# Kernel optimization log

Measured on AMD Instinct MI355X. Metric: run time of the kernel, lower is better.

Reference implementation:

```python
import jax, jax.numpy as jnp
import numpy as np

DIM_IN = 512
HIDDEN = 512
DIM_OUT = 512
BATCH = 256

def _n_tri(d):
    return (d * d + d) // 2

def _quad_expand(x):
    # x: [B, D] -> [B, D + (D^2+D)/2] with upper-triu (incl diag) pairwise products
    d = x.shape[1]
    iu0, iu1 = np.triu_indices(d)  # static indices
    x_sq = x[:, iu0] * x[:, iu1]  # [B, n_tri] -- avoids materializing full outer
    return jnp.concatenate([x, x_sq], axis=-1)

def setup_inputs() -> dict:
    key = jax.random.key(0)
    k = jax.random.split(key, 5)
    f0 = DIM_IN + _n_tri(DIM_IN)
    f1 = HIDDEN + _n_tri(HIDDEN)
    s0 = 1.0 / np.sqrt(f0)
    s1 = 1.0 / np.sqrt(f1)
    return {
        "x": jax.random.normal(k[0], (BATCH, DIM_IN), dtype=jnp.float32),
        "W0": jax.random.uniform(k[1], (HIDDEN, f0), dtype=jnp.float32, minval=-s0, maxval=s0),
        "b0": jax.random.uniform(k[2], (HIDDEN,), dtype=jnp.float32, minval=-s0, maxval=s0),
        "W1": jax.random.uniform(k[3], (DIM_OUT, f1), dtype=jnp.float32, minval=-s1, maxval=s1),
        "b1": jax.random.uniform(k[4], (DIM_OUT,), dtype=jnp.float32, minval=-s1, maxval=s1),
    }

def reference(x, W0, b0, W1, b1):
    h = _quad_expand(x) @ W0.T + b0  # [B, HIDDEN]
    out = _quad_expand(h) @ W1.T + b1  # [B, DIM_OUT]
    return out
```

## Files before the change

kernel.cpp:

```cpp
#include <hip/hip_runtime.h>

typedef short s16x8 __attribute__((ext_vector_type(8)));
typedef float f32x4 __attribute__((ext_vector_type(4)));

#define DIM     512
#define BATCH   256
#define NTRI    131328
#define FDIM    131840
#define KBLOCKS 2060
#define BN      64
#define NTILES  8
#define CCH     64

__device__ __forceinline__ unsigned short f2bf(float f) {
  __bf16 h = (__bf16)f;
  return __builtin_bit_cast(unsigned short, h);
}
__device__ __forceinline__ float bf2f(unsigned short s) {
  union { unsigned u; float f; } v; v.u = (unsigned)s << 16; return v.f;
}
__device__ __forceinline__ unsigned pk2(float a, float b) {
  return (unsigned)f2bf(a) | ((unsigned)f2bf(b) << 16);
}
__device__ __forceinline__ int swz(int m) { return (m ^ (m >> 2)) & 7; }

__global__ void setup(unsigned* __restrict__ table, const float* __restrict__ x,
                      unsigned short* __restrict__ Xt) {
  int bid = blockIdx.x;
  if (bid < 512) {
    int i = bid;
    int base = i * DIM - (i * (i - 1)) / 2;
    int len = DIM - i;
    for (int t = threadIdx.x; t < len; t += blockDim.x)
      table[base + t] = ((unsigned)i << 16) | (unsigned)(i + t);
  } else {
    int t = (bid - 512) * blockDim.x + threadIdx.x;
    int r = t & (BATCH - 1);
    int c = t >> 8;
    Xt[c * BATCH + r] = f2bf(x[r * DIM + c]);
  }
}

__global__ __launch_bounds__(512)
void featgen(const unsigned* __restrict__ table,
             const unsigned short* __restrict__ Xt,
             uint4* __restrict__ Feat)
{
  const int kb = blockIdx.x;
  const int tid = threadIdx.x;
  const int s8 = tid >> 6;
  const int lane = tid & 63;
  const int f0 = kb * 64 + s8 * 8;
  uint4* out = Feat + ((size_t)kb * 8 + s8) * 256;

  if (f0 < DIM) {
    #pragma unroll
    for (int mb = 0; mb < 4; ++mb) {
      int m = mb * 64 + lane;
      unsigned short v[8];
      #pragma unroll
      for (int e = 0; e < 8; ++e) v[e] = Xt[(f0 + e) * BATCH + m];
      uint4 pk;
      pk.x = (unsigned)v[0] | ((unsigned)v[1] << 16);
      pk.y = (unsigned)v[2] | ((unsigned)v[3] << 16);
      pk.z = (unsigned)v[4] | ((unsigned)v[5] << 16);
      pk.w = (unsigned)v[6] | ((unsigned)v[7] << 16);
      out[m] = pk;
    }
  } else {
    int p0 = f0 - DIM;
    unsigned t0 = table[p0], t7 = table[p0 + 7];
    if ((t0 >> 16) == (t7 >> 16)) {
      int i = (int)(t0 >> 16), j0 = (int)(t0 & 0xffffu);
      #pragma unroll
      for (int mb = 0; mb < 4; ++mb) {
        int m = mb * 64 + lane;
        float xi = bf2f(Xt[i * BATCH + m]);
        float pr[8];
        #pragma unroll
        for (int e = 0; e < 8; ++e) pr[e] = xi * bf2f(Xt[(j0 + e) * BATCH + m]);
        out[m] = make_uint4(pk2(pr[0], pr[1]), pk2(pr[2], pr[3]),
                            pk2(pr[4], pr[5]), pk2(pr[6], pr[7]));
      }
    } else {
      unsigned tt[8];
      #pragma unroll
      for (int e = 0; e < 8; ++e) tt[e] = table[p0 + e];
      #pragma unroll
      for (int mb = 0; mb < 4; ++mb) {
        int m = mb * 64 + lane;
        float pr[8];
        #pragma unroll
        for (int e = 0; e < 8; ++e)
          pr[e] = bf2f(Xt[(tt[e] >> 16) * BATCH + m]) * bf2f(Xt[(tt[e] & 0xffffu) * BATCH + m]);
        out[m] = make_uint4(pk2(pr[0], pr[1]), pk2(pr[2], pr[3]),
                            pk2(pr[4], pr[5]), pk2(pr[6], pr[7]));
      }
    }
  }
}

__global__ __launch_bounds__(512, 4)
void qgemm(const uint4* __restrict__ Feat,
           const float* __restrict__ W,
           unsigned short* __restrict__ partial,
           int C)
{
  __shared__ unsigned short Ws[2][4096];
  const int chunk = blockIdx.x % C;
  const int ntile = blockIdx.x / C;
  const int kb0 = (KBLOCKS * chunk) / C;
  const int kb1 = (KBLOCKS * (chunk + 1)) / C;
  const int n0 = ntile * BN;
  const int tid = threadIdx.x;
  const int lane = tid & 63;
  const int wave = tid >> 6;
  const int lm = lane & 15;
  const int lk = lane >> 4;

  const int wr0 = tid >> 4;
  const int wc16 = tid & 15;

  f32x4 acc[2][4] = {};
  f32x4 wregC[2], wregN[2], wT[2];
  uint4 afrC[2][2], afrN[2][2];

  const float* wp0 = W + (size_t)(n0 + wr0) * FDIM + wc16 * 4;
  const size_t wrow32 = (size_t)32 * FDIM;
  const int abase = lk * 256 + wave * 32 + lm;

  auto loadA = [&](uint4 (*a)[2], int kb) {
    #pragma unroll
    for (int mf = 0; mf < 2; ++mf)
      #pragma unroll
      for (int ks = 0; ks < 2; ++ks)
        a[mf][ks] = Feat[(size_t)kb * 2048 + ks * 1024 + mf * 16 + abase];
  };
  auto loadWr = [&](f32x4* w, int kb) {
    #pragma unroll
    for (int it = 0; it < 2; ++it)
      w[it] = *(const f32x4*)(wp0 + it * wrow32 + (size_t)kb * 64);
  };
  auto storeWs = [&](int buf, const f32x4* w) {
    #pragma unroll
    for (int it = 0; it < 2; ++it) {
      int r = wr0 + it * 32;
      int slot = (wc16 >> 1) ^ swz(r);
      *(uint2*)((char*)&Ws[buf][0] + r * 128 + slot * 16 + (wc16 & 1) * 8) =
          make_uint2(pk2(w[it][0], w[it][1]), pk2(w[it][2], w[it][3]));
    }
  };
  auto compute = [&](int buf, uint4 (*a)[2]) {
    #pragma unroll
    for (int ks = 0; ks < 2; ++ks) {
      s16x8 bfr[4];
      #pragma unroll
      for (int nf = 0; nf < 4; ++nf) {
        int n = nf * 16 + lm;
        int slot = (ks * 4 + lk) ^ swz(n);
        bfr[nf] = *(const s16x8*)((const char*)&Ws[buf][0] + n * 128 + slot * 16);
      }
      __builtin_amdgcn_s_setprio(1);
      #pragma unroll
      for (int mf = 0; mf < 2; ++mf)
        #pragma unroll
        for (int nf = 0; nf < 4; ++nf)
          acc[mf][nf] = __builtin_amdgcn_mfma_f32_16x16x32_bf16(
              __builtin_bit_cast(s16x8, a[mf][ks]), bfr[nf], acc[mf][nf], 0, 0, 0);
      __builtin_amdgcn_s_setprio(0);
    }
  };

  loadA(afrC, kb0);
  loadWr(wT, kb0);
  loadWr(wregC, min(kb0 + 1, KBLOCKS - 1));
  storeWs(kb0 & 1, wT);
  asm volatile("s_waitcnt lgkmcnt(0)" ::: "memory");
  __builtin_amdgcn_s_barrier();

  for (int kb = kb0; kb < kb1 - 1; ++kb) {
    const int buf = kb & 1;
    loadA(afrN, kb + 1);
    loadWr(wregN, min(kb + 2, KBLOCKS - 1));
    storeWs(buf ^ 1, wregC);
    compute(buf, afrC);
    asm volatile("s_waitcnt lgkmcnt(0)" ::: "memory");
    __builtin_amdgcn_s_barrier();
    #pragma unroll
    for (int mf = 0; mf < 2; ++mf) {
      afrC[mf][0] = afrN[mf][0]; afrC[mf][1] = afrN[mf][1];
    }
    wregC[0] = wregN[0]; wregC[1] = wregN[1];
  }

  compute((kb1 - 1) & 1, afrC);

  unsigned short* pout = partial + (size_t)chunk * (BATCH * DIM);
  #pragma unroll
  for (int mf = 0; mf < 2; ++mf) {
    #pragma unroll
    for (int nf = 0; nf < 4; ++nf) {
      int mrow = wave * 32 + mf * 16 + lk * 4;
      int ncol = n0 + nf * 16 + lm;
      #pragma unroll
      for (int r = 0; r < 4; ++r)
        pout[(size_t)(mrow + r) * DIM + ncol] = f2bf(acc[mf][nf][r]);
    }
  }
}

__global__ void reduce_h(const unsigned short* __restrict__ partial, const float* __restrict__ bias,
                         unsigned short* __restrict__ Ht, int C) {
  int u = blockIdx.x * blockDim.x + threadIdx.x;
  int t8 = u * 8;
  int b = t8 >> 9;
  int o0 = t8 & (DIM - 1);
  float s[8];
  #pragma unroll
  for (int e = 0; e < 8; ++e) s[e] = bias[o0 + e];
  for (int c = 0; c < C; ++c) {
    uint4 v = *(const uint4*)(partial + (size_t)c * (BATCH * DIM) + t8);
    unsigned w[4] = {v.x, v.y, v.z, v.w};
    #pragma unroll
    for (int p = 0; p < 4; ++p) {
      s[2*p]   += bf2f((unsigned short)(w[p] & 0xffffu));
      s[2*p+1] += bf2f((unsigned short)(w[p] >> 16));
    }
  }
  #pragma unroll
  for (int e = 0; e < 8; ++e)
    Ht[(o0 + e) * BATCH + b] = f2bf(s[e]);
}

__global__ void reduce_out(const unsigned short* __restrict__ partial, const float* __restrict__ bias,
                           float* __restrict__ out, int C) {
  int u = blockIdx.x * blockDim.x + threadIdx.x;
  int t8 = u * 8;
  int o0 = t8 & (DIM - 1);
  float s[8];
  #pragma unroll
  for (int e = 0; e < 8; ++e) s[e] = bias[o0 + e];
  for (int c = 0; c < C; ++c) {
    uint4 v = *(const uint4*)(partial + (size_t)c * (BATCH * DIM) + t8);
    unsigned w[4] = {v.x, v.y, v.z, v.w};
    #pragma unroll
    for (int p = 0; p < 4; ++p) {
      s[2*p]   += bf2f((unsigned short)(w[p] & 0xffffu));
      s[2*p+1] += bf2f((unsigned short)(w[p] >> 16));
    }
  }
  f32x4 lo = {s[0], s[1], s[2], s[3]};
  f32x4 hi = {s[4], s[5], s[6], s[7]};
  *(f32x4*)(out + t8) = lo;
  *(f32x4*)(out + t8 + 4) = hi;
}

extern "C" void kernel_launch(void* const* d_in, const int* in_sizes, int n_in,
                              void* d_out, int out_size, void* d_ws, size_t ws_size,
                              hipStream_t stream) {
  const float* x  = (const float*)d_in[0];
  const float* W0 = (const float*)d_in[1];
  const float* b0 = (const float*)d_in[2];
  const float* W1 = (const float*)d_in[3];
  const float* b1 = (const float*)d_in[4];
  float* out = (float*)d_out;

  char* ws = (char*)d_ws;
  unsigned* table    = (unsigned*)ws;
  unsigned short* Xt = (unsigned short*)(ws + 525312);
  unsigned short* Ht = (unsigned short*)(ws + 787456);
  uint4* Feat        = (uint4*)(ws + 1049600);
  size_t feat_end    = 1049600 + (size_t)KBLOCKS * 32768;
  unsigned short* partial = (unsigned short*)(ws + feat_end);

  size_t avail = (ws_size > feat_end) ? (ws_size - feat_end) : 0;
  int C = (int)(avail / ((size_t)BATCH * DIM * sizeof(unsigned short)));
  if (C > CCH) C = CCH;
  if (C < 1)  C = 1;

  setup<<<dim3(1024), dim3(256), 0, stream>>>(table, x, Xt);

  featgen<<<dim3(KBLOCKS), dim3(512), 0, stream>>>(table, Xt, Feat);
  qgemm<<<dim3(NTILES * C), dim3(512), 0, stream>>>(Feat, W0, partial, C);
  reduce_h<<<dim3(64), dim3(256), 0, stream>>>(partial, b0, Ht, C);

  featgen<<<dim3(KBLOCKS), dim3(512), 0, stream>>>(table, Ht, Feat);
  qgemm<<<dim3(NTILES * C), dim3(512), 0, stream>>>(Feat, W1, partial, C);
  reduce_out<<<dim3(64), dim3(256), 0, stream>>>(partial, b1, out, C);
}
```

Measured before the change: 243.5 us.

## Stage feature tiles into LDS via direct global-to-LDS DMA in qgemm

Reworks qgemm so the A (feature) block for each k-step is copied straight into double-buffered LDS with global_load_lds, instead of every wave loading its own fragments into registers. Workgroups grow to 1024 threads (16 waves as 8x2 over M and N), the split-K count is halved to 32 and aligned to pairs of k-blocks, and the loop is unrolled by two with explicit vmcnt/lgkmcnt waits and sched barriers. The aim is to share the A tile across waves and overlap the global loads with MFMA work. In exchange it uses more LDS, allows only one block per CU, and has fewer blocks in flight.

```diff
diff --git a/kernel.cpp b/kernel.cpp
--- a/kernel.cpp
+++ b/kernel.cpp
@@ -8,9 +8,10 @@
 #define NTRI    131328
 #define FDIM    131840
 #define KBLOCKS 2060
+#define NPAIR   1030
 #define BN      64
 #define NTILES  8
-#define CCH     64
+#define CCH     32
 
 __device__ __forceinline__ unsigned short f2bf(float f) {
   __bf16 h = (__bf16)f;
@@ -23,6 +24,13 @@
   return (unsigned)f2bf(a) | ((unsigned)f2bf(b) << 16);
 }
 __device__ __forceinline__ int swz(int m) { return (m ^ (m >> 2)) & 7; }
+
+__device__ __forceinline__ void dma16(const void* g, void* l) {
+  __builtin_amdgcn_global_load_lds(
+      (const __attribute__((address_space(1))) void*)g,
+      (__attribute__((address_space(3))) void*)l, 16, 0, 0);
+}
+#define SB() __builtin_amdgcn_sched_barrier(0)
 
 __global__ void setup(unsigned* __restrict__ table, const float* __restrict__ x,
                       unsigned short* __restrict__ Xt) {
@@ -100,108 +108,118 @@
   }
 }
 
-__global__ __launch_bounds__(512, 4)
-void qgemm(const uint4* __restrict__ Feat,
+__global__ __launch_bounds__(1024, 1)
+void qgemm(const char* __restrict__ Feat,
            const float* __restrict__ W,
            unsigned short* __restrict__ partial,
            int C)
 {
+  __shared__ char As[2][8 * 4128];
   __shared__ unsigned short Ws[2][4096];
   const int chunk = blockIdx.x % C;
   const int ntile = blockIdx.x / C;
-  const int kb0 = (KBLOCKS * chunk) / C;
-  const int kb1 = (KBLOCKS * (chunk + 1)) / C;
+  const int kb0 = 2 * ((NPAIR * chunk) / C);
+  const int kb1 = 2 * ((NPAIR * (chunk + 1)) / C);
   const int n0 = ntile * BN;
   const int tid = threadIdx.x;
   const int lane = tid & 63;
   const int wave = tid >> 6;
+  const int wm = wave & 7;
+  const int wn = wave >> 3;
   const int lm = lane & 15;
   const int lk = lane >> 4;
 
   const int wr0 = tid >> 4;
   const int wc16 = tid & 15;
 
-  f32x4 acc[2][4] = {};
-  f32x4 wregC[2], wregN[2], wT[2];
-  uint4 afrC[2][2], afrN[2][2];
+  f32x4 acc[2][2] = {};
+  f32x4 wrA, wrB;
 
   const float* wp0 = W + (size_t)(n0 + wr0) * FDIM + wc16 * 4;
-  const size_t wrow32 = (size_t)32 * FDIM;
-  const int abase = lk * 256 + wave * 32 + lm;
-
-  auto loadA = [&](uint4 (*a)[2], int kb) {
-    #pragma unroll
-    for (int mf = 0; mf < 2; ++mf)
-      #pragma unroll
-      for (int ks = 0; ks < 2; ++ks)
-        a[mf][ks] = Feat[(size_t)kb * 2048 + ks * 1024 + mf * 16 + abase];
+
+  auto dmak = [&](int kb, int buf) {
+    #pragma unroll
+    for (int p = 0; p < 2; ++p) {
+      int u = tid + p * 1024;
+      dma16(Feat + (size_t)kb * 32768 + u * 16,
+            &As[buf][(u >> 8) * 4128 + (u & 255) * 16]);
+    }
   };
-  auto loadWr = [&](f32x4* w, int kb) {
-    #pragma unroll
-    for (int it = 0; it < 2; ++it)
-      w[it] = *(const f32x4*)(wp0 + it * wrow32 + (size_t)kb * 64);
+  auto loadWr = [&](f32x4& w, int kb) {
+    w = *(const f32x4*)(wp0 + (size_t)kb * 64);
   };
-  auto storeWs = [&](int buf, const f32x4* w) {
-    #pragma unroll
-    for (int it = 0; it < 2; ++it) {
-      int r = wr0 + it * 32;
-      int slot = (wc16 >> 1) ^ swz(r);
-      *(uint2*)((char*)&Ws[buf][0] + r * 128 + slot * 16 + (wc16 & 1) * 8) =
-          make_uint2(pk2(w[it][0], w[it][1]), pk2(w[it][2], w[it][3]));
-    }
+  auto storeWs = [&](int buf, const f32x4& w) {
+    int slot = (wc16 >> 1) ^ swz(wr0);
+    *(uint2*)((char*)&Ws[buf][0] + wr0 * 128 + slot * 16 + (wc16 & 1) * 8) =
+        make_uint2(pk2(w[0], w[1]), pk2(w[2], w[3]));
   };
-  auto compute = [&](int buf, uint4 (*a)[2]) {
+  auto compute = [&](int buf) {
     #pragma unroll
     for (int ks = 0; ks < 2; ++ks) {
-      s16x8 bfr[4];
-      #pragma unroll
-      for (int nf = 0; nf < 4; ++nf) {
-        int n = nf * 16 + lm;
+      s16x8 bfr[2], afr[2];
+      #pragma unroll
+      for (int nf = 0; nf < 2; ++nf) {
+        int n = wn * 32 + nf * 16 + lm;
         int slot = (ks * 4 + lk) ^ swz(n);
         bfr[nf] = *(const s16x8*)((const char*)&Ws[buf][0] + n * 128 + slot * 16);
       }
+      #pragma unroll
+      for (int mf = 0; mf < 2; ++mf)
+        afr[mf] = *(const s16x8*)(&As[buf][(ks * 4 + lk) * 4128 + (wm * 32 + mf * 16 + lm) * 16]);
       __builtin_amdgcn_s_setprio(1);
       #pragma unroll
       for (int mf = 0; mf < 2; ++mf)
         #pragma unroll
-        for (int nf = 0; nf < 4; ++nf)
-          acc[mf][nf] = __builtin_amdgcn_mfma_f32_16x16x32_bf16(
-              __builtin_bit_cast(s16x8, a[mf][ks]), bfr[nf], acc[mf][nf], 0, 0, 0);
+        for (int nf = 0; nf < 2; ++nf)
+          acc[mf][nf] = __builtin_amdgcn_mfma_f32_16x16x32_bf16(afr[mf], bfr[nf], acc[mf][nf], 0, 0, 0);
       __builtin_amdgcn_s_setprio(0);
     }
   };
 
-  loadA(afrC, kb0);
-  loadWr(wT, kb0);
-  loadWr(wregC, min(kb0 + 1, KBLOCKS - 1));
-  storeWs(kb0 & 1, wT);
-  asm volatile("s_waitcnt lgkmcnt(0)" ::: "memory");
+  dmak(kb0, 0);
+  loadWr(wrB, kb0);
+  loadWr(wrA, kb0 + 1);
+  SB();
+  storeWs(0, wrB);
+  asm volatile("s_waitcnt lgkmcnt(0)" ::: "memory"); SB();
+  asm volatile("s_waitcnt vmcnt(1)" ::: "memory"); SB();
   __builtin_amdgcn_s_barrier();
 
-  for (int kb = kb0; kb < kb1 - 1; ++kb) {
-    const int buf = kb & 1;
-    loadA(afrN, kb + 1);
-    loadWr(wregN, min(kb + 2, KBLOCKS - 1));
-    storeWs(buf ^ 1, wregC);
-    compute(buf, afrC);
-    asm volatile("s_waitcnt lgkmcnt(0)" ::: "memory");
+  for (int kb = kb0; kb < kb1 - 2; kb += 2) {
+    dmak(kb + 1, 1);
+    loadWr(wrB, kb + 2);
+    SB();
+    storeWs(1, wrA);
+    compute(0);
+    asm volatile("s_waitcnt lgkmcnt(0)" ::: "memory"); SB();
+    asm volatile("s_waitcnt vmcnt(1)" ::: "memory"); SB();
     __builtin_amdgcn_s_barrier();
-    #pragma unroll
-    for (int mf = 0; mf < 2; ++mf) {
-      afrC[mf][0] = afrN[mf][0]; afrC[mf][1] = afrN[mf][1];
-    }
-    wregC[0] = wregN[0]; wregC[1] = wregN[1];
-  }
-
-  compute((kb1 - 1) & 1, afrC);
+    dmak(kb + 2, 0);
+    loadWr(wrA, kb + 3);
+    SB();
+    storeWs(0, wrB);
+    compute(1);
+    asm volatile("s_waitcnt lgkmcnt(0)" ::: "memory"); SB();
+    asm volatile("s_waitcnt vmcnt(1)" ::: "memory"); SB();
+    __builtin_amdgcn_s_barrier();
+  }
+
+  dmak(kb1 - 1, 1);
+  SB();
+  storeWs(1, wrA);
+  compute(0);
+  asm volatile("s_waitcnt lgkmcnt(0)" ::: "memory"); SB();
+  asm volatile("s_waitcnt vmcnt(0)" ::: "memory"); SB();
+  __builtin_amdgcn_s_barrier();
+  compute(1);
 
   unsigned short* pout = partial + (size_t)chunk * (BATCH * DIM);
   #pragma unroll
   for (int mf = 0; mf < 2; ++mf) {
     #pragma unroll
-    for (int nf = 0; nf < 4; ++nf) {
-      int mrow = wave * 32 + mf * 16 + lk * 4;
-      int ncol = n0 + nf * 16 + lm;
+    for (int nf = 0; nf < 2; ++nf) {
+      int mrow = wm * 32 + mf * 16 + lk * 4;
+      int ncol = n0 + wn * 32 + nf * 16 + lm;
       #pragma unroll
       for (int r = 0; r < 4; ++r)
         pout[(size_t)(mrow + r) * DIM + ncol] = f2bf(acc[mf][nf][r]);
@@ -269,7 +287,7 @@
   unsigned* table    = (unsigned*)ws;
   unsigned short* Xt = (unsigned short*)(ws + 525312);
   unsigned short* Ht = (unsigned short*)(ws + 787456);
-  uint4* Feat        = (uint4*)(ws + 1049600);
+  char* Feat         = ws + 1049600;
   size_t feat_end    = 1049600 + (size_t)KBLOCKS * 32768;
   unsigned short* partial = (unsigned short*)(ws + feat_end);
 
@@ -280,11 +298,11 @@
 
   setup<<<dim3(1024), dim3(256), 0, stream>>>(table, x, Xt);
 
-  featgen<<<dim3(KBLOCKS), dim3(512), 0, stream>>>(table, Xt, Feat);
-  qgemm<<<dim3(NTILES * C), dim3(512), 0, stream>>>(Feat, W0, partial, C);
+  featgen<<<dim3(KBLOCKS), dim3(512), 0, stream>>>(table, Xt, (uint4*)Feat);
+  qgemm<<<dim3(NTILES * C), dim3(1024), 0, stream>>>(Feat, W0, partial, C);
   reduce_h<<<dim3(64), dim3(256), 0, stream>>>(partial, b0, Ht, C);
 
-  featgen<<<dim3(KBLOCKS), dim3(512), 0, stream>>>(table, Ht, Feat);
-  qgemm<<<dim3(NTILES * C), dim3(512), 0, stream>>>(Feat, W1, partial, C);
+  featgen<<<dim3(KBLOCKS), dim3(512), 0, stream>>>(table, Ht, (uint4*)Feat);
+  qgemm<<<dim3(NTILES * C), dim3(1024), 0, stream>>>(Feat, W1, partial, C);
   reduce_out<<<dim3(64), dim3(256), 0, stream>>>(partial, b1, out, C);
 }
```

After: 262.0 us. 1.08x slower.

## Group four K-blocks per super-step to amortize barriers in quad GEMM

Applied to the files above, without the earlier changes.

Restructures the qgemm main loop so each iteration handles a super-block of four 64-wide K-blocks. The W tile is quadrupled in shared memory (64 KB double buffer) and W for the next super-step is loaded into registers once per step. Activation fragments are ping-ponged between two register sets across the four sub-computations. This cuts barriers and LDS store/wait phases by four and lets more global loads be in flight, at the cost of more LDS and registers, which can lower occupancy under the 512x4 launch bound.

```diff
diff --git a/kernel.cpp b/kernel.cpp
--- a/kernel.cpp
+++ b/kernel.cpp
@@ -8,6 +8,7 @@
 #define NTRI    131328
 #define FDIM    131840
 #define KBLOCKS 2060
+#define KSUP    515
 #define BN      64
 #define NTILES  8
 #define CCH     64
@@ -106,11 +107,11 @@
            unsigned short* __restrict__ partial,
            int C)
 {
-  __shared__ unsigned short Ws[2][4096];
+  __shared__ unsigned short Ws[2][16384];
   const int chunk = blockIdx.x % C;
   const int ntile = blockIdx.x / C;
-  const int kb0 = (KBLOCKS * chunk) / C;
-  const int kb1 = (KBLOCKS * (chunk + 1)) / C;
+  const int sp0 = (KSUP * chunk) / C;
+  const int sp1 = (KSUP * (chunk + 1)) / C;
   const int n0 = ntile * BN;
   const int tid = threadIdx.x;
   const int lane = tid & 63;
@@ -118,14 +119,13 @@
   const int lm = lane & 15;
   const int lk = lane >> 4;
 
-  const int wr0 = tid >> 4;
-  const int wc16 = tid & 15;
+  const int wr = tid >> 4;
+  const int wc = tid & 15;
 
   f32x4 acc[2][4] = {};
-  f32x4 wregC[2], wregN[2], wT[2];
-  uint4 afrC[2][2], afrN[2][2];
-
-  const float* wp0 = W + (size_t)(n0 + wr0) * FDIM + wc16 * 4;
+  uint4 aA[2][2], aB[2][2];
+
+  const float* wp0 = W + (size_t)(n0 + wr) * FDIM + wc * 4;
   const size_t wrow32 = (size_t)32 * FDIM;
   const int abase = lk * 256 + wave * 32 + lm;
 
@@ -136,21 +136,26 @@
       for (int ks = 0; ks < 2; ++ks)
         a[mf][ks] = Feat[(size_t)kb * 2048 + ks * 1024 + mf * 16 + abase];
   };
-  auto loadWr = [&](f32x4* w, int kb) {
-    #pragma unroll
-    for (int it = 0; it < 2; ++it)
-      w[it] = *(const f32x4*)(wp0 + it * wrow32 + (size_t)kb * 64);
+  auto loadW = [&](f32x4* w, int sp) {
+    const float* base = wp0 + (size_t)sp * 256;
+    #pragma unroll
+    for (int h = 0; h < 2; ++h)
+      #pragma unroll
+      for (int i = 0; i < 4; ++i)
+        w[h * 4 + i] = *(const f32x4*)(base + h * wrow32 + i * 64);
   };
   auto storeWs = [&](int buf, const f32x4* w) {
     #pragma unroll
-    for (int it = 0; it < 2; ++it) {
-      int r = wr0 + it * 32;
-      int slot = (wc16 >> 1) ^ swz(r);
-      *(uint2*)((char*)&Ws[buf][0] + r * 128 + slot * 16 + (wc16 & 1) * 8) =
-          make_uint2(pk2(w[it][0], w[it][1]), pk2(w[it][2], w[it][3]));
-    }
-  };
-  auto compute = [&](int buf, uint4 (*a)[2]) {
+    for (int h = 0; h < 2; ++h) {
+      int r = wr + h * 32;
+      int slot = (wc >> 1) ^ swz(r);
+      #pragma unroll
+      for (int i = 0; i < 4; ++i)
+        *(uint2*)((char*)&Ws[buf][0] + i * 8192 + r * 128 + slot * 16 + (wc & 1) * 8) =
+            make_uint2(pk2(w[h*4+i][0], w[h*4+i][1]), pk2(w[h*4+i][2], w[h*4+i][3]));
+    }
+  };
+  auto computeSub = [&](int buf, int j, const uint4 (*a)[2]) {
     #pragma unroll
     for (int ks = 0; ks < 2; ++ks) {
       s16x8 bfr[4];
@@ -158,7 +163,7 @@
       for (int nf = 0; nf < 4; ++nf) {
         int n = nf * 16 + lm;
         int slot = (ks * 4 + lk) ^ swz(n);
-        bfr[nf] = *(const s16x8*)((const char*)&Ws[buf][0] + n * 128 + slot * 16);
+        bfr[nf] = *(const s16x8*)((const char*)&Ws[buf][0] + j * 8192 + n * 128 + slot * 16);
       }
       __builtin_amdgcn_s_setprio(1);
       #pragma unroll
@@ -171,29 +176,28 @@
     }
   };
 
-  loadA(afrC, kb0);
-  loadWr(wT, kb0);
-  loadWr(wregC, min(kb0 + 1, KBLOCKS - 1));
-  storeWs(kb0 & 1, wT);
-  asm volatile("s_waitcnt lgkmcnt(0)" ::: "memory");
-  __builtin_amdgcn_s_barrier();
-
-  for (int kb = kb0; kb < kb1 - 1; ++kb) {
-    const int buf = kb & 1;
-    loadA(afrN, kb + 1);
-    loadWr(wregN, min(kb + 2, KBLOCKS - 1));
-    storeWs(buf ^ 1, wregC);
-    compute(buf, afrC);
+  {
+    f32x4 w0[8];
+    loadW(w0, sp0);
+    loadA(aA, sp0 * 4);
+    storeWs(sp0 & 1, w0);
     asm volatile("s_waitcnt lgkmcnt(0)" ::: "memory");
     __builtin_amdgcn_s_barrier();
-    #pragma unroll
-    for (int mf = 0; mf < 2; ++mf) {
-      afrC[mf][0] = afrN[mf][0]; afrC[mf][1] = afrN[mf][1];
-    }
-    wregC[0] = wregN[0]; wregC[1] = wregN[1];
-  }
-
-  compute((kb1 - 1) & 1, afrC);
+  }
+
+  for (int sp = sp0; sp < sp1; ++sp) {
+    const int buf = sp & 1;
+    const int kb = sp * 4;
+    f32x4 wn[8];
+    loadW(wn, min(sp + 1, KSUP - 1));
+    loadA(aB, kb + 1); computeSub(buf, 0, aA);
+    loadA(aA, kb + 2); computeSub(buf, 1, aB);
+    loadA(aB, kb + 3); computeSub(buf, 2, aA);
+    loadA(aA, min(kb + 4, KBLOCKS - 1)); computeSub(buf, 3, aB);
+    storeWs(buf ^ 1, wn);
+    asm volatile("s_waitcnt lgkmcnt(0)" ::: "memory");
+    __builtin_amdgcn_s_barrier();
+  }
 
   unsigned short* pout = partial + (size_t)chunk * (BATCH * DIM);
   #pragma unroll
```

Result: slower. 264.3 us (+8.5%).
